# Optimization experiments

Hardware: AMD Instinct MI355X
Metric: run time of the kernel (lower is better)

## Reference

```python
import jax, jax.numpy as jnp
import numpy as np

BS, D, H = 65536, 768, 12
DK = D // H // 2  # 32
EPS = 1e-6

def setup_inputs() -> dict:
    key = jax.random.key(0)
    ks = jax.random.split(key, 4)
    scale = 1.0 / np.sqrt(D)
    return {
        "x": jax.random.normal(ks[0], (BS, D), dtype=jnp.float32),
        "Wq": jax.random.normal(ks[1], (D, D), dtype=jnp.float32) * scale,
        "Wk": jax.random.normal(ks[2], (D, D), dtype=jnp.float32) * scale,
        "Wv": jax.random.normal(ks[3], (D, D), dtype=jnp.float32) * scale,
        "gamma": jnp.ones((D,), dtype=jnp.float32),
        "beta": jnp.zeros((D,), dtype=jnp.float32),
    }

def reference(x, Wq, Wk, Wv, gamma, beta):
    bs = x.shape[0]
    # LayerNorm (eps=1e-6)
    mu = jnp.mean(x, axis=-1, keepdims=True)
    var = jnp.mean(jnp.square(x - mu), axis=-1, keepdims=True)
    xn = (x - mu) / jnp.sqrt(var + EPS) * gamma + beta
    # QKV projections (nn.Linear, no bias: y = x @ W.T), split feature dim as (h, 2, d_k)
    q = (xn @ Wq.T).reshape(bs, H, 2, DK)
    k = (xn @ Wk.T).reshape(bs, H, 2, DK)
    v = (xn @ Wv.T).reshape(bs, H, 2, DK)
    # tiny 2x2 attention per head
    scores = jnp.einsum('bhpd,bhqd->bhpq', q, k) / np.sqrt(DK)
    attn = jax.nn.softmax(scores, axis=-1)
    out = jnp.einsum('bhpq,bhqd->bhpd', attn, v).reshape(bs, D)
    return out + x
```

## Files before the change

### kernel.cpp

```cpp
#include <hip/hip_runtime.h>

typedef _Float16 f16;
typedef _Float16 f16x8 __attribute__((ext_vector_type(8)));
typedef float f32x16 __attribute__((ext_vector_type(16)));

#define BS 65536
#define D 768
#define H 12
#define NBLK ((BS / 128) * H)
#define W_ELEMS ((size_t)D * D)
#define XN_ELEMS ((size_t)BS * D)

typedef const __attribute__((address_space(1))) void gvoid_t;
typedef __attribute__((address_space(3))) void lvoid_t;

__global__ __launch_bounds__(256, 4) void ln_kernel(const float* __restrict__ x,
                                                    const float* __restrict__ gamma,
                                                    const float* __restrict__ beta,
                                                    f16* __restrict__ xn) {
  int tid = threadIdx.x;
  int r   = tid >> 2;
  int sub = tid & 3;
  size_t row = (size_t)blockIdx.x * 64 + r;
  const float4* xr4 = (const float4*)(x + row * D) + sub * 48;
  float sum = 0.f, sq = 0.f;
#pragma unroll 8
  for (int j = 0; j < 48; ++j) {
    float4 w = xr4[j];
    sum += w.x + w.y + w.z + w.w;
    sq  += w.x * w.x + w.y * w.y + w.z * w.z + w.w * w.w;
  }
  sum += __shfl_xor(sum, 1, 64); sum += __shfl_xor(sum, 2, 64);
  sq  += __shfl_xor(sq,  1, 64); sq  += __shfl_xor(sq,  2, 64);
  float mu   = sum * (1.0f / D);
  float rstd = rsqrtf(sq * (1.0f / D) - mu * mu + 1e-6f);
  asm volatile("" ::: "memory");
  const float4* g4 = (const float4*)(gamma) + sub * 48;
  const float4* b4 = (const float4*)(beta)  + sub * 48;
  f16* xo = xn + row * D + sub * 192;
#pragma unroll 4
  for (int j = 0; j < 24; ++j) {
    float4 v0 = xr4[2 * j], v1 = xr4[2 * j + 1];
    float4 g0 = g4[2 * j],  g1 = g4[2 * j + 1];
    float4 b0 = b4[2 * j],  b1 = b4[2 * j + 1];
    f16x8 o;
    o[0] = (f16)((v0.x - mu) * rstd * g0.x + b0.x);
    o[1] = (f16)((v0.y - mu) * rstd * g0.y + b0.y);
    o[2] = (f16)((v0.z - mu) * rstd * g0.z + b0.z);
    o[3] = (f16)((v0.w - mu) * rstd * g0.w + b0.w);
    o[4] = (f16)((v1.x - mu) * rstd * g1.x + b1.x);
    o[5] = (f16)((v1.y - mu) * rstd * g1.y + b1.y);
    o[6] = (f16)((v1.z - mu) * rstd * g1.z + b1.z);
    o[7] = (f16)((v1.w - mu) * rstd * g1.w + b1.w);
    *(f16x8*)(xo + j * 8) = o;
  }
}

__global__ __launch_bounds__(256, 4) void wconv_kernel(const float* __restrict__ Wq,
                                                       const float* __restrict__ Wk,
                                                       const float* __restrict__ Wv,
                                                       f16* __restrict__ wf) {
  int b = blockIdx.x;
  int m = b / 288;
  size_t e = ((size_t)(b % 288) * 256 + threadIdx.x) * 8;
  const float* src = (m == 0 ? Wq : (m == 1 ? Wk : Wv)) + e;
  float4 v0 = *(const float4*)src;
  float4 v1 = *(const float4*)(src + 4);
  f16x8 o;
  o[0] = (f16)v0.x; o[1] = (f16)v0.y; o[2] = (f16)v0.z; o[3] = (f16)v0.w;
  o[4] = (f16)v1.x; o[5] = (f16)v1.y; o[6] = (f16)v1.z; o[7] = (f16)v1.w;
  *(f16x8*)(wf + (size_t)m * W_ELEMS + e) = o;
}

__global__ __launch_bounds__(256, 2) void qkv_attn_kernel(const f16* __restrict__ xn,
                                                          const f16* __restrict__ wf,
                                                          const float* __restrict__ x,
                                                          float* __restrict__ out) {
  __shared__ f16 sB[2][192 * 64] __attribute__((aligned(16)));

  const int tid  = threadIdx.x;
  const int wave = tid >> 6;
  const int lane = tid & 63;
  const int l31  = lane & 31;
  const int hi   = lane >> 5;

  int bid = blockIdx.x;
  int my  = (bid & 7) * (NBLK / 8) + (bid >> 3);
  int rb  = my / H;
  int h   = my % H;

  unsigned offs[6];
  {
    int rl = wave * 48 + (lane >> 3);
#pragma unroll
    for (int o = 0; o < 6; ++o) {
      int r  = rl + o * 8;
      int cc = (lane & 7) ^ ((lane >> 3) & 7);
      offs[o] = (unsigned)((r >> 6) * (int)W_ELEMS + ((h * 64 + (r & 63)) * D) + cc * 8);
    }
  }

  const int rowb = l31 * 64;
  int coff[4];
#pragma unroll
  for (int s = 0; s < 4; ++s) coff[s] = ((s * 2 + hi) ^ (l31 & 7)) * 8;

  const f16* ap = xn + ((size_t)rb * 128 + wave * 32 + l31) * D + hi * 8;

#define STAGE(KO, BUF)                                                                  \
  {                                                                                     \
    const f16* bp = wf + (KO) * 64;                                                     \
    _Pragma("unroll") for (int o = 0; o < 6; ++o) {                                     \
      __builtin_amdgcn_global_load_lds((gvoid_t*)(bp + offs[o]),                        \
                                       (lvoid_t*)(&sB[BUF][wave * 3072 + o * 512]),     \
                                       16, 0, 0);                                       \
    }                                                                                   \
  }

  STAGE(0, 0);

  f32x16 acc[6];
#pragma unroll
  for (int t = 0; t < 6; ++t)
#pragma unroll
    for (int i = 0; i < 16; ++i) acc[t][i] = 0.f;

  __syncthreads();

#pragma unroll
  for (int ko = 0; ko < 12; ++ko) {
    const int cur = ko & 1;
    if (ko < 11) STAGE(ko + 1, cur ^ 1);
    __builtin_amdgcn_sched_barrier(0);

    const f16* bb = &sB[cur][rowb];
    __builtin_amdgcn_s_setprio(1);
#pragma unroll
    for (int s = 0; s < 4; ++s) {
      f16x8 as = *(const f16x8*)(ap + ko * 64 + s * 16);
#pragma unroll
      for (int t = 0; t < 6; ++t) {
        f16x8 b = *(const f16x8*)(bb + coff[s] + t * 2048);
        acc[t] = __builtin_amdgcn_mfma_f32_32x32x16_f16(as, b, acc[t], 0, 0, 0);
      }
    }
    __builtin_amdgcn_s_setprio(0);
    if (ko < 11) __syncthreads();
  }

  {
    const size_t grow0 = (size_t)rb * 128 + wave * 32;
    const float scale = 0.17677669529663687f;
#pragma unroll
    for (int g = 0; g < 16; ++g) {
      float q0 = acc[0][g], q1 = acc[1][g];
      float k0 = acc[2][g], k1 = acc[3][g];
      float s00 = q0 * k0, s01 = q0 * k1, s10 = q1 * k0, s11 = q1 * k1;
#pragma unroll
      for (int d2 = 1; d2 <= 16; d2 <<= 1) {
        s00 += __shfl_xor(s00, d2, 64);
        s01 += __shfl_xor(s01, d2, 64);
        s10 += __shfl_xor(s10, d2, 64);
        s11 += __shfl_xor(s11, d2, 64);
      }
      s00 *= scale; s01 *= scale; s10 *= scale; s11 *= scale;
      float mx0 = fmaxf(s00, s01);
      float e00 = __expf(s00 - mx0), e01 = __expf(s01 - mx0);
      float r0 = 1.0f / (e00 + e01);
      float a00 = e00 * r0, a01 = e01 * r0;
      float mx1 = fmaxf(s10, s11);
      float e10 = __expf(s10 - mx1), e11 = __expf(s11 - mx1);
      float r1 = 1.0f / (e10 + e11);
      float a10 = e10 * r1, a11 = e11 * r1;

      int row_w = (g & 3) + 8 * (g >> 2) + 4 * hi;
      const float* xp = x   + (grow0 + row_w) * D + h * 64 + l31;
      float*       op = out + (grow0 + row_w) * D + h * 64 + l31;
      float v0 = acc[4][g], v1 = acc[5][g];
      op[0]  = a00 * v0 + a01 * v1 + xp[0];
      op[32] = a10 * v0 + a11 * v1 + xp[32];
    }
  }
#undef STAGE
}

extern "C" void kernel_launch(void* const* d_in, const int* in_sizes, int n_in,
                              void* d_out, int out_size, void* d_ws, size_t ws_size,
                              hipStream_t stream) {
  const float* x     = (const float*)d_in[0];
  const float* Wq    = (const float*)d_in[1];
  const float* Wk    = (const float*)d_in[2];
  const float* Wv    = (const float*)d_in[3];
  const float* gamma = (const float*)d_in[4];
  const float* beta  = (const float*)d_in[5];
  float* out = (float*)d_out;
  (void)in_sizes; (void)n_in; (void)out_size; (void)ws_size;

  f16* xn = (f16*)d_ws;
  f16* wf = xn + XN_ELEMS;

  ln_kernel<<<dim3(BS / 64), dim3(256), 0, stream>>>(x, gamma, beta, xn);
  wconv_kernel<<<dim3(864), dim3(256), 0, stream>>>(Wq, Wk, Wv, wf);
  qkv_attn_kernel<<<dim3(NBLK), dim3(256), 0, stream>>>(xn, wf, x, out);
}
```

Measured before the change: 772.4 us.

## Double row tile per block in QKV kernel and use one wave per row in LayerNorm

The fused QKV/attention kernel now handles 256 rows per block, with each wave computing two 32-row MFMA tiles that share every B fragment read from LDS. This halves the number of blocks and the weight-tile staging per output row. The swizzled LDS layout for B is replaced by a plain layout with new staging offsets, which may introduce LDS bank conflicts. LayerNorm is rewritten to use one wave per row with a full-wave shuffle reduction and a single pass over registers, so x is not reread. Register pressure in the main kernel roughly doubles for accumulators.

```diff
diff --git a/kernel.cpp b/kernel.cpp
--- a/kernel.cpp
+++ b/kernel.cpp
@@ -2,12 +2,14 @@
 
 typedef _Float16 f16;
 typedef _Float16 f16x8 __attribute__((ext_vector_type(8)));
+typedef _Float16 f16x4 __attribute__((ext_vector_type(4)));
 typedef float f32x16 __attribute__((ext_vector_type(16)));
 
 #define BS 65536
 #define D 768
 #define H 12
-#define NBLK ((BS / 128) * H)
+#define RB 256
+#define NBLK ((BS / RB) * H)
 #define W_ELEMS ((size_t)D * D)
 #define XN_ELEMS ((size_t)BS * D)
 
@@ -18,42 +20,43 @@
                                                     const float* __restrict__ gamma,
                                                     const float* __restrict__ beta,
                                                     f16* __restrict__ xn) {
-  int tid = threadIdx.x;
-  int r   = tid >> 2;
-  int sub = tid & 3;
-  size_t row = (size_t)blockIdx.x * 64 + r;
-  const float4* xr4 = (const float4*)(x + row * D) + sub * 48;
-  float sum = 0.f, sq = 0.f;
-#pragma unroll 8
-  for (int j = 0; j < 48; ++j) {
-    float4 w = xr4[j];
-    sum += w.x + w.y + w.z + w.w;
-    sq  += w.x * w.x + w.y * w.y + w.z * w.z + w.w * w.w;
-  }
-  sum += __shfl_xor(sum, 1, 64); sum += __shfl_xor(sum, 2, 64);
-  sq  += __shfl_xor(sq,  1, 64); sq  += __shfl_xor(sq,  2, 64);
+  int wave = threadIdx.x >> 6, lane = threadIdx.x & 63;
+  size_t row = (size_t)blockIdx.x * 4 + wave;
+  const float4* xr = (const float4*)(x + row * D) + lane * 3;
+  float4 v0 = xr[0], v1 = xr[1], v2 = xr[2];
+  float sum = (v0.x + v0.y) + (v0.z + v0.w) + (v1.x + v1.y) + (v1.z + v1.w)
+            + (v2.x + v2.y) + (v2.z + v2.w);
+  float sq = v0.x*v0.x + v0.y*v0.y + v0.z*v0.z + v0.w*v0.w
+           + v1.x*v1.x + v1.y*v1.y + v1.z*v1.z + v1.w*v1.w
+           + v2.x*v2.x + v2.y*v2.y + v2.z*v2.z + v2.w*v2.w;
+#pragma unroll
+  for (int d2 = 1; d2 <= 32; d2 <<= 1) {
+    sum += __shfl_xor(sum, d2, 64);
+    sq  += __shfl_xor(sq,  d2, 64);
+  }
   float mu   = sum * (1.0f / D);
   float rstd = rsqrtf(sq * (1.0f / D) - mu * mu + 1e-6f);
-  asm volatile("" ::: "memory");
-  const float4* g4 = (const float4*)(gamma) + sub * 48;
-  const float4* b4 = (const float4*)(beta)  + sub * 48;
-  f16* xo = xn + row * D + sub * 192;
-#pragma unroll 4
-  for (int j = 0; j < 24; ++j) {
-    float4 v0 = xr4[2 * j], v1 = xr4[2 * j + 1];
-    float4 g0 = g4[2 * j],  g1 = g4[2 * j + 1];
-    float4 b0 = b4[2 * j],  b1 = b4[2 * j + 1];
-    f16x8 o;
-    o[0] = (f16)((v0.x - mu) * rstd * g0.x + b0.x);
-    o[1] = (f16)((v0.y - mu) * rstd * g0.y + b0.y);
-    o[2] = (f16)((v0.z - mu) * rstd * g0.z + b0.z);
-    o[3] = (f16)((v0.w - mu) * rstd * g0.w + b0.w);
-    o[4] = (f16)((v1.x - mu) * rstd * g1.x + b1.x);
-    o[5] = (f16)((v1.y - mu) * rstd * g1.y + b1.y);
-    o[6] = (f16)((v1.z - mu) * rstd * g1.z + b1.z);
-    o[7] = (f16)((v1.w - mu) * rstd * g1.w + b1.w);
-    *(f16x8*)(xo + j * 8) = o;
-  }
+  const float4* g4 = (const float4*)(gamma) + lane * 3;
+  const float4* b4 = (const float4*)(beta)  + lane * 3;
+  float4 g0 = g4[0], g1 = g4[1], g2 = g4[2];
+  float4 b0 = b4[0], b1 = b4[1], b2 = b4[2];
+  f16* xo = xn + row * D + lane * 12;
+  f16x4 o0, o1, o2;
+  o0[0] = (f16)((v0.x - mu) * rstd * g0.x + b0.x);
+  o0[1] = (f16)((v0.y - mu) * rstd * g0.y + b0.y);
+  o0[2] = (f16)((v0.z - mu) * rstd * g0.z + b0.z);
+  o0[3] = (f16)((v0.w - mu) * rstd * g0.w + b0.w);
+  o1[0] = (f16)((v1.x - mu) * rstd * g1.x + b1.x);
+  o1[1] = (f16)((v1.y - mu) * rstd * g1.y + b1.y);
+  o1[2] = (f16)((v1.z - mu) * rstd * g1.z + b1.z);
+  o1[3] = (f16)((v1.w - mu) * rstd * g1.w + b1.w);
+  o2[0] = (f16)((v2.x - mu) * rstd * g2.x + b2.x);
+  o2[1] = (f16)((v2.y - mu) * rstd * g2.y + b2.y);
+  o2[2] = (f16)((v2.z - mu) * rstd * g2.z + b2.z);
+  o2[3] = (f16)((v2.w - mu) * rstd * g2.w + b2.w);
+  *(f16x4*)(xo)     = o0;
+  *(f16x4*)(xo + 4) = o1;
+  *(f16x4*)(xo + 8) = o2;
 }
 
 __global__ __launch_bounds__(256, 4) void wconv_kernel(const float* __restrict__ Wq,
@@ -91,39 +94,39 @@
 
   unsigned offs[6];
   {
-    int rl = wave * 48 + (lane >> 3);
+    int rl = wave * 48 + (lane & 7);
+    int c  = lane >> 3;
 #pragma unroll
     for (int o = 0; o < 6; ++o) {
-      int r  = rl + o * 8;
-      int cc = (lane & 7) ^ ((lane >> 3) & 7);
-      offs[o] = (unsigned)((r >> 6) * (int)W_ELEMS + ((h * 64 + (r & 63)) * D) + cc * 8);
+      int r = rl + o * 8;
+      offs[o] = (unsigned)((r >> 6) * (int)W_ELEMS + (h * 64 + (r & 63)) * D + c * 8);
     }
   }
 
-  const int rowb = l31 * 64;
-  int coff[4];
-#pragma unroll
-  for (int s = 0; s < 4; ++s) coff[s] = ((s * 2 + hi) ^ (l31 & 7)) * 8;
-
-  const f16* ap = xn + ((size_t)rb * 128 + wave * 32 + l31) * D + hi * 8;
-
-#define STAGE(KO, BUF)                                                                  \
-  {                                                                                     \
-    const f16* bp = wf + (KO) * 64;                                                     \
-    _Pragma("unroll") for (int o = 0; o < 6; ++o) {                                     \
-      __builtin_amdgcn_global_load_lds((gvoid_t*)(bp + offs[o]),                        \
-                                       (lvoid_t*)(&sB[BUF][wave * 3072 + o * 512]),     \
-                                       16, 0, 0);                                       \
-    }                                                                                   \
+  const int rbase = (l31 >> 3) * 512 + hi * 64 + (l31 & 7) * 8;
+
+  const f16* ap0 = xn + ((size_t)rb * RB + wave * 64 + l31) * D + hi * 8;
+  const f16* ap1 = ap0 + (size_t)32 * D;
+
+#define STAGE(KO, BUF)                                                                   \
+  {                                                                                      \
+    const f16* bp = wf + (KO) * 64;                                                      \
+    _Pragma("unroll") for (int o = 0; o < 6; ++o) {                                      \
+      __builtin_amdgcn_global_load_lds((gvoid_t*)(bp + offs[o]),                         \
+                                       (lvoid_t*)(&sB[BUF][(wave * 6 + o) * 512]),       \
+                                       16, 0, 0);                                        \
+    }                                                                                    \
   }
 
   STAGE(0, 0);
 
-  f32x16 acc[6];
+  f32x16 acc[6][2];
 #pragma unroll
   for (int t = 0; t < 6; ++t)
 #pragma unroll
-    for (int i = 0; i < 16; ++i) acc[t][i] = 0.f;
+    for (int rt = 0; rt < 2; ++rt)
+#pragma unroll
+      for (int i = 0; i < 16; ++i) acc[t][rt][i] = 0.f;
 
   __syncthreads();
 
@@ -133,15 +136,17 @@
     if (ko < 11) STAGE(ko + 1, cur ^ 1);
     __builtin_amdgcn_sched_barrier(0);
 
-    const f16* bb = &sB[cur][rowb];
+    const f16* bb = &sB[cur][rbase];
     __builtin_amdgcn_s_setprio(1);
 #pragma unroll
     for (int s = 0; s < 4; ++s) {
-      f16x8 as = *(const f16x8*)(ap + ko * 64 + s * 16);
+      f16x8 a0 = *(const f16x8*)(ap0 + ko * 64 + s * 16);
+      f16x8 a1 = *(const f16x8*)(ap1 + ko * 64 + s * 16);
 #pragma unroll
       for (int t = 0; t < 6; ++t) {
-        f16x8 b = *(const f16x8*)(bb + coff[s] + t * 2048);
-        acc[t] = __builtin_amdgcn_mfma_f32_32x32x16_f16(as, b, acc[t], 0, 0, 0);
+        f16x8 b = *(const f16x8*)(bb + t * 2048 + s * 128);
+        acc[t][0] = __builtin_amdgcn_mfma_f32_32x32x16_f16(a0, b, acc[t][0], 0, 0, 0);
+        acc[t][1] = __builtin_amdgcn_mfma_f32_32x32x16_f16(a1, b, acc[t][1], 0, 0, 0);
       }
     }
     __builtin_amdgcn_s_setprio(0);
@@ -149,36 +154,39 @@
   }
 
   {
-    const size_t grow0 = (size_t)rb * 128 + wave * 32;
     const float scale = 0.17677669529663687f;
 #pragma unroll
-    for (int g = 0; g < 16; ++g) {
-      float q0 = acc[0][g], q1 = acc[1][g];
-      float k0 = acc[2][g], k1 = acc[3][g];
-      float s00 = q0 * k0, s01 = q0 * k1, s10 = q1 * k0, s11 = q1 * k1;
-#pragma unroll
-      for (int d2 = 1; d2 <= 16; d2 <<= 1) {
-        s00 += __shfl_xor(s00, d2, 64);
-        s01 += __shfl_xor(s01, d2, 64);
-        s10 += __shfl_xor(s10, d2, 64);
-        s11 += __shfl_xor(s11, d2, 64);
+    for (int rt = 0; rt < 2; ++rt) {
+      const size_t grow0 = (size_t)rb * RB + wave * 64 + rt * 32;
+#pragma unroll
+      for (int g = 0; g < 16; ++g) {
+        float q0 = acc[0][rt][g], q1 = acc[1][rt][g];
+        float k0 = acc[2][rt][g], k1 = acc[3][rt][g];
+        float s00 = q0 * k0, s01 = q0 * k1, s10 = q1 * k0, s11 = q1 * k1;
+#pragma unroll
+        for (int d2 = 1; d2 <= 16; d2 <<= 1) {
+          s00 += __shfl_xor(s00, d2, 64);
+          s01 += __shfl_xor(s01, d2, 64);
+          s10 += __shfl_xor(s10, d2, 64);
+          s11 += __shfl_xor(s11, d2, 64);
+        }
+        s00 *= scale; s01 *= scale; s10 *= scale; s11 *= scale;
+        float mx0 = fmaxf(s00, s01);
+        float e00 = __expf(s00 - mx0), e01 = __expf(s01 - mx0);
+        float r0 = 1.0f / (e00 + e01);
+        float a00 = e00 * r0, a01 = e01 * r0;
+        float mx1 = fmaxf(s10, s11);
+        float e10 = __expf(s10 - mx1), e11 = __expf(s11 - mx1);
+        float r1 = 1.0f / (e10 + e11);
+        float a10 = e10 * r1, a11 = e11 * r1;
+
+        int row_w = (g & 3) + 8 * (g >> 2) + 4 * hi;
+        const float* xp = x   + (grow0 + row_w) * D + h * 64 + l31;
+        float*       op = out + (grow0 + row_w) * D + h * 64 + l31;
+        float v0 = acc[4][rt][g], v1 = acc[5][rt][g];
+        op[0]  = a00 * v0 + a01 * v1 + xp[0];
+        op[32] = a10 * v0 + a11 * v1 + xp[32];
       }
-      s00 *= scale; s01 *= scale; s10 *= scale; s11 *= scale;
-      float mx0 = fmaxf(s00, s01);
-      float e00 = __expf(s00 - mx0), e01 = __expf(s01 - mx0);
-      float r0 = 1.0f / (e00 + e01);
-      float a00 = e00 * r0, a01 = e01 * r0;
-      float mx1 = fmaxf(s10, s11);
-      float e10 = __expf(s10 - mx1), e11 = __expf(s11 - mx1);
-      float r1 = 1.0f / (e10 + e11);
-      float a10 = e10 * r1, a11 = e11 * r1;
-
-      int row_w = (g & 3) + 8 * (g >> 2) + 4 * hi;
-      const float* xp = x   + (grow0 + row_w) * D + h * 64 + l31;
-      float*       op = out + (grow0 + row_w) * D + h * 64 + l31;
-      float v0 = acc[4][g], v1 = acc[5][g];
-      op[0]  = a00 * v0 + a01 * v1 + xp[0];
-      op[32] = a10 * v0 + a11 * v1 + xp[32];
     }
   }
 #undef STAGE
@@ -199,7 +207,7 @@
   f16* xn = (f16*)d_ws;
   f16* wf = xn + XN_ELEMS;
 
-  ln_kernel<<<dim3(BS / 64), dim3(256), 0, stream>>>(x, gamma, beta, xn);
+  ln_kernel<<<dim3(BS / 4), dim3(256), 0, stream>>>(x, gamma, beta, xn);
   wconv_kernel<<<dim3(864), dim3(256), 0, stream>>>(Wq, Wk, Wv, wf);
   qkv_attn_kernel<<<dim3(NBLK), dim3(256), 0, stream>>>(xn, wf, x, out);
 }
```

Measured after the change: 712.6 us. 1.08x faster.
